# Optimization experiments

Hardware: AMD Instinct MI355X
Metric: run time of the kernel (lower is better)

## Reference

```python
import jax, jax.numpy as jnp
import numpy as np

N_SRC = 100000
N_DST = 50000
N_EDGES = 600000
D = 128


def setup_inputs() -> dict:
    key = jax.random.key(0)
    k1, k2, k3, k4, k5 = jax.random.split(key, 5)
    src_rep = jax.random.normal(k1, (N_SRC, D), dtype=jnp.float32)
    dst_rep = jax.random.normal(k2, (N_DST, D), dtype=jnp.float32)
    edge_src = jax.random.randint(k3, (N_EDGES,), 0, N_SRC, dtype=jnp.int64)
    edge_dst = jax.random.randint(k4, (N_EDGES,), 0, N_DST, dtype=jnp.int64)
    W = jax.random.normal(k5, (2 * D, D), dtype=jnp.float32) * (1.0 / np.sqrt(2 * D))
    b = jnp.zeros((D,), dtype=jnp.float32)
    return {"src_rep": src_rep, "dst_rep": dst_rep, "edge_src": edge_src,
            "edge_dst": edge_dst, "W": W, "b": b}


def reference(src_rep, dst_rep, edge_src, edge_dst, W, b):
    # copy_src: gather source reps along edges  [E, D]
    msgs = src_rep[edge_src]
    # sum reduce: scatter-add messages to destination nodes  [N_dst, D]
    agg = jax.ops.segment_sum(msgs, edge_dst, num_segments=dst_rep.shape[0])
    # NodeUpdater: concat(dst rep, summed messages) -> Linear -> activation
    # (Dropout is identity in eval mode.)
    concat = jnp.concatenate([dst_rep, agg], axis=1)  # [N_dst, 2D]
    new_rep = jax.nn.relu(concat @ W + b)  # [N_dst, D]
    return new_rep
```

## Files before the change

kernel.cpp:

```cpp
#include <hip/hip_runtime.h>

#define N_SRC   100000
#define N_DST   50000
#define N_EDGES 600000
#define D       128
#define RPB     16
#define PAD     48

#define CONV_BLOCKS  ((N_SRC * D / 4) / 256)
#define MISC_ELEMS   (2 * D * D + N_DST + D)
#define MISC_BLOCKS  ((MISC_ELEMS + 255) / 256)
#define FILL_BLOCKS  ((N_EDGES / 2 + 255) / 256)

typedef short bf16x8 __attribute__((ext_vector_type(8)));
typedef float f32x4  __attribute__((ext_vector_type(4)));

static __device__ __forceinline__ unsigned short f2bf(float f) {
    unsigned u = __float_as_uint(f);
    u += 0x7FFF + ((u >> 16) & 1);
    return (unsigned short)(u >> 16);
}
static __device__ __forceinline__ unsigned pk(float a, float b) {
    return (unsigned)f2bf(a) | ((unsigned)f2bf(b) << 16);
}
static __device__ __forceinline__ void addpk(float* a, uint4 u) {
    a[0] += __uint_as_float(u.x << 16);
    a[1] += __uint_as_float(u.x & 0xFFFF0000u);
    a[2] += __uint_as_float(u.y << 16);
    a[3] += __uint_as_float(u.y & 0xFFFF0000u);
    a[4] += __uint_as_float(u.z << 16);
    a[5] += __uint_as_float(u.z & 0xFFFF0000u);
    a[6] += __uint_as_float(u.w << 16);
    a[7] += __uint_as_float(u.w & 0xFFFF0000u);
}

__global__ __launch_bounds__(256) void prep_kernel(
    const float* __restrict__ src_rep, unsigned short* __restrict__ srcb,
    const float* __restrict__ W, unsigned short* __restrict__ Wt,
    int* __restrict__ cnt) {
    if (blockIdx.x < CONV_BLOCKS) {
        size_t t = (size_t)blockIdx.x * 256 + threadIdx.x;
        float4 v = reinterpret_cast<const float4*>(src_rep)[t];
        uint2 w;
        w.x = pk(v.x, v.y); w.y = pk(v.z, v.w);
        reinterpret_cast<uint2*>(srcb)[t] = w;
    } else {
        int t = (blockIdx.x - CONV_BLOCKS) * 256 + threadIdx.x;
        if (t < 2 * D * D) {
            int n = t >> 8, k = t & 255;
            Wt[n * 256 + k] = f2bf(W[(size_t)k * D + n]);
        }
        int c = t - 2 * D * D;
        if (c >= 0 && c < N_DST) cnt[c] = 0;
        int z = c - N_DST;
        if (z >= 0 && z < D) srcb[(size_t)N_SRC * D + z] = 0;
    }
}

__global__ __launch_bounds__(256) void fill_kernel(
    const int* __restrict__ edge_src, const int* __restrict__ edge_dst,
    int* __restrict__ cnt, int* __restrict__ perm) {
    int e0 = (blockIdx.x * 256 + threadIdx.x) * 2;
    if (e0 < N_EDGES) {
        int2 s2 = *reinterpret_cast<const int2*>(edge_src + e0);
        int2 d2 = *reinterpret_cast<const int2*>(edge_dst + e0);
        int p0 = atomicAdd(&cnt[d2.x], 1);
        if (p0 < PAD) perm[d2.x * PAD + p0] = s2.x;
        int p1 = atomicAdd(&cnt[d2.y], 1);
        if (p1 < PAD) perm[d2.y * PAD + p1] = s2.y;
    }
}

__global__ __launch_bounds__(512) void fused_kernel(
    const unsigned short* __restrict__ srcb,
    const float* __restrict__ dst_rep,
    const int*   __restrict__ cnt,
    const int*   __restrict__ perm,
    const unsigned short* __restrict__ Wt,
    const float* __restrict__ bias,
    float*       __restrict__ out) {
    __shared__ __align__(16) unsigned short stage[8][2][2][512];
    __shared__ unsigned short Abf[16 * 256];
    const int row0 = blockIdx.x * 16;
    const int tid = threadIdx.x, lane = tid & 63, wave = tid >> 6;
    const int q = lane >> 4, cl = lane & 15;

    const int dn0 = row0 + wave * 2;
    const int2 cc = *reinterpret_cast<const int2*>(&cnt[dn0]);
    const int dmA = min(cc.x, PAD) - 1, dmB = min(cc.y, PAD) - 1;
    const int dcA = max(dmA, 0), dcB = max(dmB, 0);
    const int piA = perm[(size_t)dn0 * PAD + min(lane, PAD - 1)];
    const int piB = perm[(size_t)(dn0 + 1) * PAD + min(lane, PAD - 1)];
    const int rounds = (max(dmA, dmB) + 4) >> 2;

    if (tid < 256) {
        int r = tid >> 4, b = tid & 15;
        const float4* p = reinterpret_cast<const float4*>(
            dst_rep + (size_t)(row0 + r) * D + b * 8);
        float4 v0 = p[0], v1 = p[1];
        uint4 w;
        w.x = pk(v0.x, v0.y); w.y = pk(v0.z, v0.w);
        w.z = pk(v1.x, v1.y); w.w = pk(v1.z, v1.w);
        *reinterpret_cast<uint4*>(&Abf[r * 256 + (b ^ (r & 7)) * 8]) = w;
    }

    float accA[8] = {}, accB[8] = {};
    auto ISSUE = [&](int rd, int slot) {
        int e = rd * 4 + q;
        int rA = __shfl(piA, min(e, dcA)); rA = (e <= dmA) ? rA : N_SRC;
        int rB = __shfl(piB, min(e, dcB)); rB = (e <= dmB) ? rB : N_SRC;
        __builtin_amdgcn_global_load_lds(
            (const unsigned int*)(srcb + (size_t)rA * D + cl * 8),
            (unsigned int*)(&stage[wave][slot][0][0]), 16, 0, 0);
        __builtin_amdgcn_global_load_lds(
            (const unsigned int*)(srcb + (size_t)rB * D + cl * 8),
            (unsigned int*)(&stage[wave][slot][1][0]), 16, 0, 0);
    };
    auto CONSUME = [&](int slot) {
        uint4 uA = *reinterpret_cast<const uint4*>(&stage[wave][slot][0][q * 128 + cl * 8]);
        uint4 uB = *reinterpret_cast<const uint4*>(&stage[wave][slot][1][q * 128 + cl * 8]);
        addpk(accA, uA); addpk(accB, uB);
    };

    if (rounds > 0) {
        ISSUE(0, 0);
        for (int rd = 0; rd + 1 < rounds; ++rd) {
            ISSUE(rd + 1, (rd + 1) & 1);
            asm volatile("s_waitcnt vmcnt(2)" ::: "memory");
            __builtin_amdgcn_sched_barrier(0);
            CONSUME(rd & 1);
            asm volatile("s_waitcnt lgkmcnt(0)" ::: "memory");
            __builtin_amdgcn_sched_barrier(0);
        }
        asm volatile("s_waitcnt vmcnt(0)" ::: "memory");
        __builtin_amdgcn_sched_barrier(0);
        CONSUME((rounds - 1) & 1);
    }

#pragma unroll
    for (int i = 0; i < 8; ++i) {
        accA[i] += __shfl_xor(accA[i], 16);
        accA[i] += __shfl_xor(accA[i], 32);
        accB[i] += __shfl_xor(accB[i], 16);
        accB[i] += __shfl_xor(accB[i], 32);
    }
    if (lane < 16) {
        const int rA = wave * 2, rB = wave * 2 + 1;
        uint4 w0, w1;
        w0.x = pk(accA[0], accA[1]); w0.y = pk(accA[2], accA[3]);
        w0.z = pk(accA[4], accA[5]); w0.w = pk(accA[6], accA[7]);
        w1.x = pk(accB[0], accB[1]); w1.y = pk(accB[2], accB[3]);
        w1.z = pk(accB[4], accB[5]); w1.w = pk(accB[6], accB[7]);
        *reinterpret_cast<uint4*>(&Abf[rA * 256 + ((16 + cl) ^ (rA & 7)) * 8]) = w0;
        *reinterpret_cast<uint4*>(&Abf[rB * 256 + ((16 + cl) ^ (rB & 7)) * 8]) = w1;
    }
    __syncthreads();

    f32x4 c0 = {0.f, 0.f, 0.f, 0.f};
    const int ar = lane & 15;
    const int kb = lane >> 4;
    const int n0 = wave * 16 + (lane & 15);
#pragma unroll
    for (int s = 0; s < 8; ++s) {
        int b = s * 4 + kb;
        bf16x8 af = *reinterpret_cast<const bf16x8*>(&Abf[ar * 256 + (b ^ (ar & 7)) * 8]);
        bf16x8 b0 = *reinterpret_cast<const bf16x8*>(&Wt[(size_t)n0 * 256 + s * 32 + kb * 8]);
        c0 = __builtin_amdgcn_mfma_f32_16x16x32_bf16(af, b0, c0, 0, 0, 0);
    }

    const float bv = bias[n0];
#pragma unroll
    for (int g = 0; g < 4; ++g) {
        size_t orow = row0 + (lane >> 4) * 4 + g;
        out[orow * D + n0] = fmaxf(c0[g] + bv, 0.f);
    }
}

__global__ __launch_bounds__(256) void prep_small_kernel(
    const float* __restrict__ W, unsigned short* __restrict__ Wt,
    int* __restrict__ cnt) {
    int t = blockIdx.x * 256 + threadIdx.x;
    if (t < 2 * D * D) {
        int n = t >> 8, k = t & 255;
        Wt[n * 256 + k] = f2bf(W[(size_t)k * D + n]);
    }
    int c = t - 2 * D * D;
    if (c >= 0 && c < N_DST) cnt[c] = 0;
}

__global__ __launch_bounds__(256) void gather_f32_kernel(
    const float* __restrict__ src_rep,
    const int*   __restrict__ cnt,
    const int*   __restrict__ perm,
    unsigned short* __restrict__ agg) {
    const int tid = threadIdx.x, lane = tid & 63, wave = tid >> 6;
    const int h = lane >> 5, c = lane & 31;
    const int dn = blockIdx.x * 4 + wave;
    const int deg = min(cnt[dn], PAD);
    const int pi = perm[(size_t)dn * PAD + min(lane, PAD - 1)];

    f32x4 a0 = {0.f, 0.f, 0.f, 0.f}, a1 = a0, a2 = a0, a3 = a0;
    const int dm1 = deg - 1;
    for (int base = 0; base < deg; base += 8) {
        int e0 = base + h, e1 = base + 2 + h, e2 = base + 4 + h, e3 = base + 6 + h;
        int s0 = __shfl(pi, min(e0, max(dm1, 0)));
        int s1 = __shfl(pi, min(e1, max(dm1, 0)));
        int s2 = __shfl(pi, min(e2, max(dm1, 0)));
        int s3 = __shfl(pi, min(e3, max(dm1, 0)));
        if (e0 <= dm1) a0 += *reinterpret_cast<const f32x4*>(src_rep + (size_t)s0 * D + c * 4);
        if (e1 <= dm1) a1 += *reinterpret_cast<const f32x4*>(src_rep + (size_t)s1 * D + c * 4);
        if (e2 <= dm1) a2 += *reinterpret_cast<const f32x4*>(src_rep + (size_t)s2 * D + c * 4);
        if (e3 <= dm1) a3 += *reinterpret_cast<const f32x4*>(src_rep + (size_t)s3 * D + c * 4);
    }
    a0 += a1; a2 += a3; a0 += a2;
#pragma unroll
    for (int qq = 0; qq < 4; ++qq) a0[qq] += __shfl_xor(a0[qq], 32);
    if (h == 0) {
        uint2 w;
        w.x = pk(a0[0], a0[1]); w.y = pk(a0[2], a0[3]);
        *reinterpret_cast<uint2*>(agg + (size_t)dn * D + c * 4) = w;
    }
}

__global__ __launch_bounds__(256) void gemm_kernel(
    const float* __restrict__ dst_rep,
    const unsigned short* __restrict__ agg,
    const unsigned short* __restrict__ Wt,
    const float* __restrict__ bias,
    float*       __restrict__ out) {
    __shared__ unsigned short Abf[RPB * 2 * D];
    const int row0 = blockIdx.x * RPB;
    const int tid = threadIdx.x, lane = tid & 63, wave = tid >> 6;
    {
        int r = tid >> 4, b = tid & 15;
        const float4* p = reinterpret_cast<const float4*>(
            dst_rep + (size_t)(row0 + r) * D + b * 8);
        float4 v0 = p[0], v1 = p[1];
        uint4 w;
        w.x = pk(v0.x, v0.y); w.y = pk(v0.z, v0.w);
        w.z = pk(v1.x, v1.y); w.w = pk(v1.z, v1.w);
        *reinterpret_cast<uint4*>(&Abf[r * 256 + (b ^ (r & 7)) * 8]) = w;
        uint4 g = *reinterpret_cast<const uint4*>(agg + (size_t)(row0 + r) * D + b * 8);
        *reinterpret_cast<uint4*>(&Abf[r * 256 + ((16 + b) ^ (r & 7)) * 8]) = g;
    }
    __syncthreads();

    f32x4 c0 = {0.f, 0.f, 0.f, 0.f}, c1 = {0.f, 0.f, 0.f, 0.f};
    const int ar = lane & 15;
    const int kb = lane >> 4;
    const int n0 = wave * 32 + (lane & 15);
#pragma unroll
    for (int s = 0; s < 8; ++s) {
        int b = s * 4 + kb;
        bf16x8 af = *reinterpret_cast<const bf16x8*>(&Abf[ar * 256 + (b ^ (ar & 7)) * 8]);
        int kbase = s * 32 + kb * 8;
        bf16x8 b0 = *reinterpret_cast<const bf16x8*>(&Wt[(size_t)n0 * 256 + kbase]);
        bf16x8 b1 = *reinterpret_cast<const bf16x8*>(&Wt[(size_t)(n0 + 16) * 256 + kbase]);
        c0 = __builtin_amdgcn_mfma_f32_16x16x32_bf16(af, b0, c0, 0, 0, 0);
        c1 = __builtin_amdgcn_mfma_f32_16x16x32_bf16(af, b1, c1, 0, 0, 0);
    }
    const float bv0 = bias[wave * 32 + (lane & 15)];
    const float bv1 = bias[wave * 32 + 16 + (lane & 15)];
#pragma unroll
    for (int g = 0; g < 4; ++g) {
        size_t orow = row0 + (lane >> 4) * 4 + g;
        out[orow * D + wave * 32 + (lane & 15)]      = fmaxf(c0[g] + bv0, 0.f);
        out[orow * D + wave * 32 + 16 + (lane & 15)] = fmaxf(c1[g] + bv1, 0.f);
    }
}

extern "C" void kernel_launch(void* const* d_in, const int* in_sizes, int n_in,
                              void* d_out, int out_size, void* d_ws, size_t ws_size,
                              hipStream_t stream) {
    const float* src_rep  = (const float*)d_in[0];
    const float* dst_rep  = (const float*)d_in[1];
    const int*   edge_src = (const int*)d_in[2];
    const int*   edge_dst = (const int*)d_in[3];
    const float* W        = (const float*)d_in[4];
    const float* bias     = (const float*)d_in[5];
    float*       out      = (float*)d_out;

    int* cnt  = (int*)d_ws;
    int* perm = cnt + N_DST;
    size_t wt_off = (((size_t)N_DST * (1 + PAD) * 4 + 255) / 256) * 256;
    unsigned short* Wt   = (unsigned short*)((char*)d_ws + wt_off);
    unsigned short* big  = Wt + (size_t)2 * D * D;
    const size_t need_full = wt_off + ((size_t)2 * D * D + (size_t)(N_SRC + 1) * D)
                             * sizeof(unsigned short);

    if (ws_size >= need_full) {
        unsigned short* srcb = big;
        prep_kernel<<<CONV_BLOCKS + MISC_BLOCKS, 256, 0, stream>>>(
            src_rep, srcb, W, Wt, cnt);
        fill_kernel<<<FILL_BLOCKS, 256, 0, stream>>>(edge_src, edge_dst, cnt, perm);
        fused_kernel<<<N_DST / 16, 512, 0, stream>>>(
            srcb, dst_rep, cnt, perm, Wt, bias, out);
    } else {
        unsigned short* agg = big;
        prep_small_kernel<<<MISC_BLOCKS, 256, 0, stream>>>(W, Wt, cnt);
        fill_kernel<<<FILL_BLOCKS, 256, 0, stream>>>(edge_src, edge_dst, cnt, perm);
        gather_f32_kernel<<<N_DST / 4, 256, 0, stream>>>(src_rep, cnt, perm, agg);
        gemm_kernel<<<N_DST / RPB, 256, 0, stream>>>(dst_rep, agg, Wt, bias, out);
    }
}
```

Baseline: 98.53 us.

## Deepen gather pipeline to four in-flight async LDS loads per wave

The per-wave gather of neighbor source rows moves from a double-buffered scheme, with two loads per round, to a four-slot ring of single async global-to-LDS loads that alternate between the two destination rows. The first four loads are issued before the dst_rep conversion into LDS, so that conversion overlaps the memory latency. The aim is to keep more loads in flight and hide gather latency. In exchange, every wave now runs at least two chunks (rows padded with the dummy N_SRC row) even for low-degree nodes, which adds redundant loads.

```diff
diff --git a/kernel.cpp b/kernel.cpp
--- a/kernel.cpp
+++ b/kernel.cpp
@@ -79,7 +79,7 @@
     const unsigned short* __restrict__ Wt,
     const float* __restrict__ bias,
     float*       __restrict__ out) {
-    __shared__ __align__(16) unsigned short stage[8][2][2][512];
+    __shared__ __align__(16) unsigned short stage[8][4][512];
     __shared__ unsigned short Abf[16 * 256];
     const int row0 = blockIdx.x * 16;
     const int tid = threadIdx.x, lane = tid & 63, wave = tid >> 6;
@@ -91,7 +91,31 @@
     const int dcA = max(dmA, 0), dcB = max(dmB, 0);
     const int piA = perm[(size_t)dn0 * PAD + min(lane, PAD - 1)];
     const int piB = perm[(size_t)(dn0 + 1) * PAD + min(lane, PAD - 1)];
-    const int rounds = (max(dmA, dmB) + 4) >> 2;
+    const int degM = max(dmA, dmB) + 1;
+    const int C = max((degM + 3) >> 2, 2);
+    const int R = 2 * C;
+
+    float accA[8] = {}, accB[8] = {};
+    auto ISSUE = [&](int i) {
+        const int p = i & 1, c = i >> 1;
+        const int e = c * 4 + q;
+        int srow;
+        if (p == 0) { srow = __shfl(piA, min(e, dcA)); srow = (e <= dmA) ? srow : N_SRC; }
+        else        { srow = __shfl(piB, min(e, dcB)); srow = (e <= dmB) ? srow : N_SRC; }
+        __builtin_amdgcn_global_load_lds(
+            (const unsigned int*)(srcb + (size_t)srow * D + cl * 8),
+            (unsigned int*)(&stage[wave][i & 3][0]), 16, 0, 0);
+    };
+    auto CONSUME_A = [&](int i) {
+        uint4 u = *reinterpret_cast<const uint4*>(&stage[wave][i & 3][lane * 8]);
+        addpk(accA, u);
+    };
+    auto CONSUME_B = [&](int i) {
+        uint4 u = *reinterpret_cast<const uint4*>(&stage[wave][i & 3][lane * 8]);
+        addpk(accB, u);
+    };
+
+    ISSUE(0); ISSUE(1); ISSUE(2); ISSUE(3);
 
     if (tid < 256) {
         int r = tid >> 4, b = tid & 15;
@@ -104,38 +128,32 @@
         *reinterpret_cast<uint4*>(&Abf[r * 256 + (b ^ (r & 7)) * 8]) = w;
     }
 
-    float accA[8] = {}, accB[8] = {};
-    auto ISSUE = [&](int rd, int slot) {
-        int e = rd * 4 + q;
-        int rA = __shfl(piA, min(e, dcA)); rA = (e <= dmA) ? rA : N_SRC;
-        int rB = __shfl(piB, min(e, dcB)); rB = (e <= dmB) ? rB : N_SRC;
-        __builtin_amdgcn_global_load_lds(
-            (const unsigned int*)(srcb + (size_t)rA * D + cl * 8),
-            (unsigned int*)(&stage[wave][slot][0][0]), 16, 0, 0);
-        __builtin_amdgcn_global_load_lds(
-            (const unsigned int*)(srcb + (size_t)rB * D + cl * 8),
-            (unsigned int*)(&stage[wave][slot][1][0]), 16, 0, 0);
-    };
-    auto CONSUME = [&](int slot) {
-        uint4 uA = *reinterpret_cast<const uint4*>(&stage[wave][slot][0][q * 128 + cl * 8]);
-        uint4 uB = *reinterpret_cast<const uint4*>(&stage[wave][slot][1][q * 128 + cl * 8]);
-        addpk(accA, uA); addpk(accB, uB);
-    };
-
-    if (rounds > 0) {
-        ISSUE(0, 0);
-        for (int rd = 0; rd + 1 < rounds; ++rd) {
-            ISSUE(rd + 1, (rd + 1) & 1);
-            asm volatile("s_waitcnt vmcnt(2)" ::: "memory");
-            __builtin_amdgcn_sched_barrier(0);
-            CONSUME(rd & 1);
-            asm volatile("s_waitcnt lgkmcnt(0)" ::: "memory");
-            __builtin_amdgcn_sched_barrier(0);
-        }
-        asm volatile("s_waitcnt vmcnt(0)" ::: "memory");
+    for (int i = 0; i < R - 4; i += 2) {
+        asm volatile("s_waitcnt vmcnt(3)" ::: "memory");
         __builtin_amdgcn_sched_barrier(0);
-        CONSUME((rounds - 1) & 1);
-    }
+        CONSUME_A(i);
+        asm volatile("s_waitcnt lgkmcnt(0)" ::: "memory");
+        __builtin_amdgcn_sched_barrier(0);
+        ISSUE(i + 4);
+        asm volatile("s_waitcnt vmcnt(3)" ::: "memory");
+        __builtin_amdgcn_sched_barrier(0);
+        CONSUME_B(i + 1);
+        asm volatile("s_waitcnt lgkmcnt(0)" ::: "memory");
+        __builtin_amdgcn_sched_barrier(0);
+        ISSUE(i + 5);
+    }
+    asm volatile("s_waitcnt vmcnt(3)" ::: "memory");
+    __builtin_amdgcn_sched_barrier(0);
+    CONSUME_A(R - 4);
+    asm volatile("s_waitcnt vmcnt(2)" ::: "memory");
+    __builtin_amdgcn_sched_barrier(0);
+    CONSUME_B(R - 3);
+    asm volatile("s_waitcnt vmcnt(1)" ::: "memory");
+    __builtin_amdgcn_sched_barrier(0);
+    CONSUME_A(R - 2);
+    asm volatile("s_waitcnt vmcnt(0)" ::: "memory");
+    __builtin_amdgcn_sched_barrier(0);
+    CONSUME_B(R - 1);
 
 #pragma unroll
     for (int i = 0; i < 8; ++i) {
```

Result: slower. 100.6 us (+2.1%).
